# Kernel tuning notes

Hardware: AMD Instinct MI355X
Metric: run time of the kernel (lower is better)

The kernel has to match this reference:

```python
import jax, jax.numpy as jnp
import numpy as np

B, A, T, D, H, ATTN = 32, 128, 96, 16, 128, 64
MAX_DIST, EMB = 50, 32


def _ln(x, g, b, eps=1e-5):
    m = x.mean(-1, keepdims=True)
    v = ((x - m) ** 2).mean(-1, keepdims=True)
    return (x - m) / jnp.sqrt(v + eps) * g + b


def _lstm_layer(xs, Wih, Whh, bih, bhh):
    # xs: (N, T, Din); PyTorch gate order i, f, g, o
    n = xs.shape[0]
    h0 = jnp.zeros((n, Whh.shape[1]), xs.dtype)
    bias = bih + bhh
    def step(carry, x_t):
        h, c = carry
        gates = x_t @ Wih.T + h @ Whh.T + bias
        i, f, g, o = jnp.split(gates, 4, axis=-1)
        c = jax.nn.sigmoid(f) * c + jax.nn.sigmoid(i) * jnp.tanh(g)
        h = jax.nn.sigmoid(o) * jnp.tanh(c)
        return (h, c), h
    _, hs = jax.lax.scan(step, (h0, h0), jnp.swapaxes(xs, 0, 1))
    return jnp.swapaxes(hs, 0, 1)  # (N, T, H)


def _forward(ranks, x, W_ih0, W_hh0, b_ih0, b_hh0, W_ih1, W_hh1, b_ih1, b_hh1,
             attn_w, attn_W1, attn_W2, ln1_g, ln1_b, proj_W, proj_b,
             Wq, bq, Wk, bk, Wv, bv, rank_emb, rw1_W, rw1_b, rw2_W,
             ff1_W, ff1_b, ff2_W, ff2_b, ln2_g, ln2_b, sp1_W, sp1_b, sp2_W, sp2_b):
    b, a, t, d = x.shape
    xs = x.reshape(b * a, t, d)
    # LSTM-HA (dropout disabled, eval mode)
    h1 = _lstm_layer(xs, W_ih0, W_hh0, b_ih0, b_hh0)
    h2 = _lstm_layer(h1, W_ih1, W_hh1, b_ih1, b_hh1)
    hT = h2[:, -1, :]
    # additive history attention, vectorized over all timesteps
    alpha = jnp.tanh(h2 @ attn_W1 + (hT @ attn_W2)[:, None, :]) @ attn_w  # (b*a, t)
    w = jax.nn.softmax(alpha, axis=1)
    ctx = jnp.einsum('nt,nth->nh', w, h2)
    rep = _ln(ctx, ln1_g, ln1_b).reshape(b, a, -1)  # (b, a, H)
    # CAAN
    xp = rep @ proj_W + proj_b
    q = xp @ Wq + bq
    k = xp @ Wk + bk
    v = xp @ Wv + bv
    scores = jnp.einsum('bnd,bmd->bnm', q, k) / (ATTN ** 0.5)
    dist = jnp.clip(jnp.abs(ranks[:, :, None] - ranks[:, None, :]), 0, MAX_DIST)
    emb = rank_emb[dist]  # (b, a, a, EMB)
    gate = jax.nn.sigmoid(jax.nn.relu(emb @ rw1_W + rw1_b) @ rw2_W)  # (b, a, a)
    attn = jax.nn.softmax(scores * gate, axis=-1)
    ao = jnp.einsum('bnm,bmd->bnd', attn, v)
    ff = _ln(jax.nn.relu(ao @ ff1_W + ff1_b) @ ff2_W + ff2_b, ln2_g, ln2_b)
    return jax.nn.sigmoid((jax.nn.relu(ff @ sp1_W + sp1_b) @ sp2_W + sp2_b)[..., 0])


def setup_inputs() -> dict:
    key = jax.random.key(0)
    ks = jax.random.split(key, 40)
    it = iter(range(40))
    def rn(shape, s):
        return jax.random.normal(ks[next(it)], shape, jnp.float32) * s
    sH = 1.0 / float(np.sqrt(H))
    sA = 1.0 / float(np.sqrt(ATTN))
    return dict(
        x=jax.random.normal(ks[next(it)], (B, A, T, D), jnp.float32),
        ranks=jax.random.randint(ks[next(it)], (B, A), 0, A),
        W_ih0=rn((4 * H, D), sH), W_hh0=rn((4 * H, H), sH),
        b_ih0=jnp.zeros(4 * H), b_hh0=jnp.zeros(4 * H),
        W_ih1=rn((4 * H, H), sH), W_hh1=rn((4 * H, H), sH),
        b_ih1=jnp.zeros(4 * H), b_hh1=jnp.zeros(4 * H),
        attn_w=rn((H,), 0.06), attn_W1=rn((H, H), sH), attn_W2=rn((H, H), sH),
        ln1_g=jnp.ones(H), ln1_b=jnp.zeros(H),
        proj_W=rn((H, ATTN), sH), proj_b=jnp.zeros(ATTN),
        Wq=rn((ATTN, ATTN), sA), bq=jnp.zeros(ATTN),
        Wk=rn((ATTN, ATTN), sA), bk=jnp.zeros(ATTN),
        Wv=rn((ATTN, ATTN), sA), bv=jnp.zeros(ATTN),
        rank_emb=rn((MAX_DIST + 1, EMB), 1.0),
        rw1_W=rn((EMB, 16), 1.0 / float(np.sqrt(EMB))), rw1_b=jnp.zeros(16),
        rw2_W=rn((16,), 0.25),
        ff1_W=rn((ATTN, 2 * ATTN), sA), ff1_b=jnp.zeros(2 * ATTN),
        ff2_W=rn((2 * ATTN, ATTN), 1.0 / float(np.sqrt(2 * ATTN))), ff2_b=jnp.zeros(ATTN),
        ln2_g=jnp.ones(ATTN), ln2_b=jnp.zeros(ATTN),
        sp1_W=rn((ATTN, 32), sA), sp1_b=jnp.zeros(32),
        sp2_W=rn((32, 1), 0.18), sp2_b=jnp.zeros(1),
    )


def reference(x, ranks, W_ih0, W_hh0, b_ih0, b_hh0, W_ih1, W_hh1, b_ih1, b_hh1,
              attn_w, attn_W1, attn_W2, ln1_g, ln1_b, proj_W, proj_b,
              Wq, bq, Wk, bk, Wv, bv, rank_emb, rw1_W, rw1_b, rw2_W,
              ff1_W, ff1_b, ff2_W, ff2_b, ln2_g, ln2_b, sp1_W, sp1_b, sp2_W, sp2_b):
    return _forward(ranks, x, W_ih0, W_hh0, b_ih0, b_hh0, W_ih1, W_hh1, b_ih1, b_hh1,
                    attn_w, attn_W1, attn_W2, ln1_g, ln1_b, proj_W, proj_b,
                    Wq, bq, Wk, bk, Wv, bv, rank_emb, rw1_W, rw1_b, rw2_W,
                    ff1_W, ff1_b, ff2_W, ff2_b, ln2_g, ln2_b, sp1_W, sp1_b, sp2_W, sp2_b)
```

## Files before the change

kernel.cpp:

```cpp
#include <hip/hip_runtime.h>
#include <hip/hip_bf16.h>

namespace {

constexpr int T_ = 96;
constexpr int H_ = 128;

typedef short s8v __attribute__((ext_vector_type(8)));
typedef float f4v __attribute__((ext_vector_type(4)));

__device__ __forceinline__ float rcp_(float x) { return __builtin_amdgcn_rcpf(x); }
__device__ __forceinline__ float sig_(float x) { return rcp_(1.f + __expf(-x)); }
__device__ __forceinline__ float tanh_(float x) { return 1.f - 2.f * rcp_(__expf(2.f * x) + 1.f); }

__device__ __forceinline__ unsigned short bf16u(float f) {
  union { float f; unsigned u; } v; v.f = f;
  unsigned r = v.u + 0x7FFFu + ((v.u >> 16) & 1u);
  return (unsigned short)(r >> 16);
}
__device__ __forceinline__ float bf2f(unsigned short b) {
  union { unsigned u; float f; } v; v.u = ((unsigned)b) << 16;
  return v.f;
}

__device__ __forceinline__ s8v load8(const float* __restrict__ p) {
  const float4 a = *reinterpret_cast<const float4*>(p);
  const float4 b = *reinterpret_cast<const float4*>(p + 4);
  s8v r;
  r[0] = (short)bf16u(a.x); r[1] = (short)bf16u(a.y);
  r[2] = (short)bf16u(a.z); r[3] = (short)bf16u(a.w);
  r[4] = (short)bf16u(b.x); r[5] = (short)bf16u(b.y);
  r[6] = (short)bf16u(b.z); r[7] = (short)bf16u(b.w);
  return r;
}

__device__ __forceinline__ f4v mfma16(s8v a, s8v b, f4v c) {
  return __builtin_amdgcn_mfma_f32_16x16x32_bf16(a, b, c, 0, 0, 0);
}

__device__ __forceinline__ void barrier_lds() {
  __builtin_amdgcn_sched_barrier(0);
  asm volatile("s_waitcnt lgkmcnt(0)" ::: "memory");
  __builtin_amdgcn_s_barrier();
  __builtin_amdgcn_sched_barrier(0);
}

__global__ __launch_bounds__(64) void k0_gate(
    const float* __restrict__ remb,
    const float* __restrict__ rw1W, const float* __restrict__ rw1b,
    const float* __restrict__ rw2W,
    float* __restrict__ glut)
{
  const int d = threadIdx.x;
  if (d > 50) return;
  const float* er = remb + d * 32;
  float g = 0.f;
#pragma unroll
  for (int e = 0; e < 16; ++e) {
    float hs = rw1b[e];
#pragma unroll 8
    for (int i = 0; i < 32; ++i) hs += er[i] * rw1W[i * 16 + e];
    g += fmaxf(hs, 0.f) * rw2W[e];
  }
  glut[d] = sig_(g);
}

__global__ __launch_bounds__(256) void k0_w1(
    const float* __restrict__ W1, unsigned short* __restrict__ w1f)
{
  const int e = blockIdx.x * 256 + threadIdx.x;
  const int k = e >> 7, nn = e & 127;
  const int f = ((((nn >> 4) * 4 + (k >> 5)) * 4 + ((k >> 3) & 3)) * 16 + (nn & 15)) * 8 + (k & 7);
  w1f[f] = bf16u(W1[e]);
}

__global__ __launch_bounds__(256) void k0_whh1(
    const float* __restrict__ Whh1, unsigned short* __restrict__ whh1f)
{
  const int e = blockIdx.x * 256 + threadIdx.x;
  const int n = e >> 7, k = e & 127;
  const int g = n >> 7, wv = (n >> 4) & 7, l16 = n & 15;
  const int kt = k >> 5, lq = (k >> 3) & 3, i = k & 7;
  const int dst = (((g * 8 + wv) * 4 + kt) * 64 + lq * 16 + l16) * 8 + i;
  whh1f[dst] = bf16u(Whh1[e]);
}

__global__ __launch_bounds__(512) void k1_lstm_mfma(
    const float* __restrict__ x,
    const float* __restrict__ Wih0, const float* __restrict__ Whh0,
    const float* __restrict__ bih0, const float* __restrict__ bhh0,
    const float* __restrict__ Wih1, const float* __restrict__ whh1f,
    const float* __restrict__ bih1, const float* __restrict__ bhh1,
    unsigned short* __restrict__ hist)
{
  __shared__ __align__(16) unsigned short w1l[512 * 128];
  __shared__ __align__(16) unsigned short h1s[2][16 * 128];
  __shared__ __align__(16) unsigned short h2s[2][16 * 128];
  __shared__ __align__(16) unsigned short xb[2][16 * 32];

  const int tid  = threadIdx.x;
  const int lane = tid & 63;
  const int wv   = tid >> 6;
  const int l16  = lane & 15;
  const int lq   = lane >> 4;
  const int seqbase = blockIdx.x * 16;

  for (int i = tid; i < 2 * 16 * 128; i += 512) {
    (&h1s[0][0])[i] = 0; (&h2s[0][0])[i] = 0;
  }
  if (tid < 256) {
    const int s = tid >> 4, d = tid & 15;
    xb[0][s * 32 + 16 + d] = 0; xb[1][s * 32 + 16 + d] = 0;
    xb[0][s * 32 + d] = bf16u(x[((size_t)(seqbase + s) * T_ + 0) * 16 + d]);
  }
  {
    const uint4* src = reinterpret_cast<const uint4*>(whh1f);
    uint4* dst = reinterpret_cast<uint4*>(w1l);
    for (int i = tid; i < 8192; i += 512) dst[i] = src[i];
  }

  s8v whh0[4][4], wih1[4][4], wx0[4];
  float b0[4], b1[4];
  int wb[4];
#pragma unroll
  for (int g = 0; g < 4; ++g) {
    const int gr = g * 128 + 16 * wv + l16;
    b0[g] = bih0[gr] + bhh0[gr];
    b1[g] = bih1[gr] + bhh1[gr];
    wb[g] = ((g * 8 + wv) * 4) * 1024 + lane * 16;
#pragma unroll
    for (int kt = 0; kt < 4; ++kt) {
      const int k0 = kt * 32 + lq * 8;
      whh0[g][kt] = load8(Whh0 + (size_t)gr * 128 + k0);
      wih1[g][kt] = load8(Wih1 + (size_t)gr * 128 + k0);
    }
    if (lq < 2) wx0[g] = load8(Wih0 + (size_t)gr * 16 + lq * 8);
    else { s8v z; for (int i2 = 0; i2 < 8; ++i2) z[i2] = 0; wx0[g] = z; }
  }

  float c1[4] = {0.f, 0.f, 0.f, 0.f}, c2[4] = {0.f, 0.f, 0.f, 0.f};
  int cur = 0;
  __syncthreads();

  const int sw = (l16 & 7) << 4;
  const int hunit = 16 * wv + l16;

  for (int t = 0; t < T_; ++t) {
    const int xc = t & 1;
    float xv = 0.f;
    const bool xpf = (t + 1 < T_) && (tid < 256);
    if (xpf) {
      const int s = tid >> 4, d = tid & 15;
      xv = x[((size_t)(seqbase + s) * T_ + (t + 1)) * 16 + d];
    }

    f4v acc[4];
#pragma unroll
    for (int g = 0; g < 4; ++g) acc[g] = f4v{b0[g], b0[g], b0[g], b0[g]};
    {
      const s8v ax = *reinterpret_cast<const s8v*>(
          reinterpret_cast<const char*>(&xb[xc][0]) + l16 * 64 + lq * 16);
#pragma unroll
      for (int g = 0; g < 4; ++g) acc[g] = mfma16(ax, wx0[g], acc[g]);
    }
#pragma unroll
    for (int kt = 0; kt < 4; ++kt) {
      const s8v ah = *reinterpret_cast<const s8v*>(
          reinterpret_cast<const char*>(&h1s[cur][0]) + l16 * 256 +
          ((kt * 64 + lq * 16) ^ sw));
#pragma unroll
      for (int g = 0; g < 4; ++g) acc[g] = mfma16(ah, whh0[g][kt], acc[g]);
    }
#pragma unroll
    for (int ss = 0; ss < 4; ++ss) {
      const int seq = lq * 4 + ss;
      const float iv = sig_(acc[0][ss]);
      const float fv = sig_(acc[1][ss]);
      const float gv = tanh_(acc[2][ss]);
      const float ov = sig_(acc[3][ss]);
      c1[ss] = fv * c1[ss] + iv * gv;
      const float hv = ov * tanh_(c1[ss]);
      *reinterpret_cast<unsigned short*>(
          reinterpret_cast<char*>(&h1s[cur ^ 1][0]) + seq * 256 +
          ((2 * hunit) ^ ((seq & 7) << 4))) = bf16u(hv);
    }
    barrier_lds();

#pragma unroll
    for (int g = 0; g < 4; ++g) acc[g] = f4v{b1[g], b1[g], b1[g], b1[g]};
#pragma unroll
    for (int kt = 0; kt < 4; ++kt) {
      const int ko = (kt * 64 + lq * 16) ^ sw;
      const s8v a1 = *reinterpret_cast<const s8v*>(
          reinterpret_cast<const char*>(&h1s[cur ^ 1][0]) + l16 * 256 + ko);
      const s8v a2 = *reinterpret_cast<const s8v*>(
          reinterpret_cast<const char*>(&h2s[cur][0]) + l16 * 256 + ko);
#pragma unroll
      for (int g = 0; g < 4; ++g) {
        acc[g] = mfma16(a1, wih1[g][kt], acc[g]);
        const s8v bw = *reinterpret_cast<const s8v*>(
            reinterpret_cast<const char*>(w1l) + wb[g] + kt * 1024);
        acc[g] = mfma16(a2, bw, acc[g]);
      }
    }
#pragma unroll
    for (int ss = 0; ss < 4; ++ss) {
      const int seq = lq * 4 + ss;
      const float iv = sig_(acc[0][ss]);
      const float fv = sig_(acc[1][ss]);
      const float gv = tanh_(acc[2][ss]);
      const float ov = sig_(acc[3][ss]);
      c2[ss] = fv * c2[ss] + iv * gv;
      const float hv = ov * tanh_(c2[ss]);
      *reinterpret_cast<unsigned short*>(
          reinterpret_cast<char*>(&h2s[cur ^ 1][0]) + seq * 256 +
          ((2 * hunit) ^ ((seq & 7) << 4))) = bf16u(hv);
    }
    if (xpf) {
      const int s = tid >> 4, d = tid & 15;
      xb[xc ^ 1][s * 32 + d] = bf16u(xv);
    }
    barrier_lds();

    {
      const int seq = tid >> 5;
      const int u0  = (tid & 31) * 4;
      const uint2 v = *reinterpret_cast<const uint2*>(
          reinterpret_cast<const char*>(&h2s[cur ^ 1][0]) + seq * 256 +
          ((2 * u0) ^ ((seq & 7) << 4)));
      *reinterpret_cast<uint2*>(
          hist + ((size_t)(seqbase + seq) * T_ + t) * H_ + u0) = v;
    }
    cur ^= 1;
  }
}

__global__ __launch_bounds__(384, 2) void k2_pool_mfma(
    const unsigned short* __restrict__ hist,
    const unsigned short* __restrict__ w1f,
    const float* __restrict__ attn_w,
    const float* __restrict__ W2,
    const float* __restrict__ ln1g, const float* __restrict__ ln1b,
    float* __restrict__ rep)
{
  __shared__ __align__(16) unsigned short hst[96 * 128];
  __shared__ float sS[128], aws[128], alpha[96], wts[96], red[128], hTs[128];
  __shared__ float ctxP[3][128];

  const int n = blockIdx.x;
  const int tid = threadIdx.x;
  const int lane = tid & 63;
  const int wv = tid >> 6;
  const int l16 = lane & 15;
  const int lq = lane >> 4;

  const unsigned short* hsrc = hist + (size_t)n * T_ * H_;
  for (int i = tid; i < 1536; i += 384) {
    const int row = i >> 4, c16 = i & 15;
    const uint4 v = *reinterpret_cast<const uint4*>(hsrc + row * 128 + c16 * 8);
    *reinterpret_cast<uint4*>(
        reinterpret_cast<char*>(hst) + row * 256 + ((c16 * 16) ^ ((row & 7) << 4))) = v;
  }
  if (tid < 128) aws[tid] = attn_w[tid];
  __syncthreads();

  if (tid < 128) hTs[tid] = bf2f(hst[95 * 128 + (tid ^ 56)]);
  __syncthreads();
  if (tid < 128) {
    float s = 0.f;
    for (int h = 0; h < 128; ++h) s += hTs[h] * W2[(size_t)h * 128 + tid];
    sS[tid] = s;
  }
  __syncthreads();

  {
    const int row0 = wv * 16 + l16;
    f4v acc[8];
#pragma unroll
    for (int nt = 0; nt < 8; ++nt) acc[nt] = f4v{0.f, 0.f, 0.f, 0.f};
#pragma unroll
    for (int kt = 0; kt < 4; ++kt) {
      const s8v a = *reinterpret_cast<const s8v*>(
          reinterpret_cast<const char*>(hst) + row0 * 256 +
          ((kt * 64 + lq * 16) ^ ((row0 & 7) << 4)));
#pragma unroll
      for (int nt = 0; nt < 8; ++nt) {
        const s8v b = *reinterpret_cast<const s8v*>(
            w1f + ((((nt << 2) + kt) << 2 | lq) * 16 + l16) * 8);
        acc[nt] = mfma16(a, b, acc[nt]);
      }
    }
    float pa[4] = {0.f, 0.f, 0.f, 0.f};
#pragma unroll
    for (int nt = 0; nt < 8; ++nt) {
      const int col = nt * 16 + l16;
      const float ss = sS[col], aw = aws[col];
#pragma unroll
      for (int i2 = 0; i2 < 4; ++i2) pa[i2] += tanh_(acc[nt][i2] + ss) * aw;
    }
#pragma unroll
    for (int i2 = 0; i2 < 4; ++i2) {
      float v = pa[i2];
      v += __shfl_xor(v, 8); v += __shfl_xor(v, 4);
      v += __shfl_xor(v, 2); v += __shfl_xor(v, 1);
      if (l16 == 0) alpha[wv * 16 + lq * 4 + i2] = v;
    }
  }
  __syncthreads();

  if (tid < 128) red[tid] = (tid < 96) ? alpha[tid] : -1e30f;
  __syncthreads();
  for (int sft = 64; sft > 0; sft >>= 1) {
    if (tid < sft) red[tid] = fmaxf(red[tid], red[tid + sft]);
    __syncthreads();
  }
  const float mx = red[0];
  __syncthreads();
  if (tid < 128) {
    const float e = (tid < 96) ? __expf(alpha[tid] - mx) : 0.f;
    red[tid] = e;
    if (tid < 96) wts[tid] = e;
  }
  __syncthreads();
  for (int sft = 64; sft > 0; sft >>= 1) {
    if (tid < sft) red[tid] += red[tid + sft];
    __syncthreads();
  }
  const float inv = rcp_(red[0]);
  if (tid < 96) wts[tid] *= inv;
  __syncthreads();

  {
    const int th = tid >> 7, j = tid & 127;
    float cp = 0.f;
    for (int t = th * 32; t < th * 32 + 32; ++t)
      cp += wts[t] * bf2f(hst[t * 128 + (j ^ ((t & 7) << 3))]);
    ctxP[th][j] = cp;
  }
  __syncthreads();
  if (tid < 128) {
    hTs[tid] = ctxP[0][tid] + ctxP[1][tid] + ctxP[2][tid];
    red[tid] = hTs[tid];
  }
  __syncthreads();
  for (int sft = 64; sft > 0; sft >>= 1) {
    if (tid < sft) red[tid] += red[tid + sft];
    __syncthreads();
  }
  const float mean = red[0] * (1.f / 128.f);
  __syncthreads();
  if (tid < 128) { const float d = hTs[tid] - mean; red[tid] = d * d; }
  __syncthreads();
  for (int sft = 64; sft > 0; sft >>= 1) {
    if (tid < sft) red[tid] += red[tid + sft];
    __syncthreads();
  }
  const float var = red[0] * (1.f / 128.f);
  if (tid < 128)
    rep[(size_t)n * H_ + tid] =
        (hTs[tid] - mean) * rsqrtf(var + 1e-5f) * ln1g[tid] + ln1b[tid];
}

__global__ __launch_bounds__(256) void k3_qkv(
    const float* __restrict__ rep,
    const float* __restrict__ projW, const float* __restrict__ projb,
    const float* __restrict__ Wq, const float* __restrict__ bq,
    const float* __restrict__ Wk, const float* __restrict__ bk,
    const float* __restrict__ Wv, const float* __restrict__ bv,
    float* __restrict__ q, float* __restrict__ k, float* __restrict__ v)
{
  const int rbase = blockIdx.x * 32;
  const int tid = threadIdx.x;
  __shared__ float reps[32][128];
  __shared__ float xps[32][64];
  for (int i = tid; i < 32 * 128; i += 256)
    reps[i >> 7][i & 127] = rep[(size_t)(rbase + (i >> 7)) * 128 + (i & 127)];
  __syncthreads();
  const int col = tid & 63, rg = tid >> 6;
#pragma unroll 2
  for (int rr = 0; rr < 8; ++rr) {
    const int r = rg * 8 + rr;
    float acc = projb[col];
    for (int kk = 0; kk < 128; ++kk) acc += reps[r][kk] * projW[kk * 64 + col];
    xps[r][col] = acc;
  }
  __syncthreads();
#pragma unroll 2
  for (int rr = 0; rr < 8; ++rr) {
    const int r = rg * 8 + rr;
    float aq = bq[col], ak = bk[col], av = bv[col];
    for (int kk = 0; kk < 64; ++kk) {
      const float xv = xps[r][kk];
      aq += xv * Wq[kk * 64 + col];
      ak += xv * Wk[kk * 64 + col];
      av += xv * Wv[kk * 64 + col];
    }
    const size_t o = (size_t)(rbase + r) * 64 + col;
    q[o] = aq; k[o] = ak; v[o] = av;
  }
}

__global__ __launch_bounds__(128) void k4_attn(
    const float* __restrict__ q, const float* __restrict__ kbuf, const float* __restrict__ vbuf,
    const int* __restrict__ ranks, const float* __restrict__ glut,
    float* __restrict__ ao)
{
  const int bn = blockIdx.x;
  const int b = bn >> 7;
  const int m = threadIdx.x;
  __shared__ float qs[64], attnw[128], red[128], aoP[2][64], gl[51];
  if (m < 64) qs[m] = q[(size_t)bn * 64 + m];
  if (m >= 64 && m < 64 + 51) gl[m - 64] = glut[m - 64];
  __syncthreads();
  const float* kr = kbuf + (size_t)(b * 128 + m) * 64;
  float sc = 0.f;
#pragma unroll 8
  for (int d = 0; d < 64; ++d) sc += qs[d] * kr[d];
  sc *= 0.125f;
  const int rn = ranks[bn], rm = ranks[b * 128 + m];
  int dist = rn - rm;
  if (dist < 0) dist = -dist;
  if (dist > 50) dist = 50;
  const float smv = sc * gl[dist];
  red[m] = smv;
  __syncthreads();
  for (int sft = 64; sft > 0; sft >>= 1) {
    if (m < sft) red[m] = fmaxf(red[m], red[m + sft]);
    __syncthreads();
  }
  const float mx = red[0];
  __syncthreads();
  const float e = __expf(smv - mx);
  red[m] = e;
  __syncthreads();
  for (int sft = 64; sft > 0; sft >>= 1) {
    if (m < sft) red[m] += red[m + sft];
    __syncthreads();
  }
  attnw[m] = e / red[0];
  __syncthreads();
  const int d = m & 63, half = m >> 6;
  float acc = 0.f;
  for (int mm = half * 64; mm < half * 64 + 64; ++mm)
    acc += attnw[mm] * vbuf[(size_t)(b * 128 + mm) * 64 + d];
  aoP[half][d] = acc;
  __syncthreads();
  if (m < 64) ao[(size_t)bn * 64 + m] = aoP[0][m] + aoP[1][m];
}

__global__ __launch_bounds__(128) void k5_ffout(
    const float* __restrict__ ao,
    const float* __restrict__ ff1W, const float* __restrict__ ff1b,
    const float* __restrict__ ff2W, const float* __restrict__ ff2b,
    const float* __restrict__ ln2g, const float* __restrict__ ln2b,
    const float* __restrict__ sp1W, const float* __restrict__ sp1b,
    const float* __restrict__ sp2W, const float* __restrict__ sp2b,
    float* __restrict__ out)
{
  const int row = blockIdx.x;
  const int tid = threadIdx.x;
  __shared__ float aos[64], hid[128], ffs[64], red[128], h2b[32];
  if (tid < 64) aos[tid] = ao[(size_t)row * 64 + tid];
  __syncthreads();
  float hv = ff1b[tid];
  for (int dd = 0; dd < 64; ++dd) hv += aos[dd] * ff1W[dd * 128 + tid];
  hid[tid] = fmaxf(hv, 0.f);
  __syncthreads();
  float yv = 0.f;
  if (tid < 64) {
    yv = ff2b[tid];
    for (int h2 = 0; h2 < 128; ++h2) yv += hid[h2] * ff2W[h2 * 64 + tid];
  }
  red[tid] = (tid < 64) ? yv : 0.f;
  __syncthreads();
  for (int sft = 64; sft > 0; sft >>= 1) {
    if (tid < sft) red[tid] += red[tid + sft];
    __syncthreads();
  }
  const float mean = red[0] * (1.f / 64.f);
  __syncthreads();
  {
    const float d2 = (tid < 64) ? (yv - mean) : 0.f;
    red[tid] = d2 * d2;
  }
  __syncthreads();
  for (int sft = 64; sft > 0; sft >>= 1) {
    if (tid < sft) red[tid] += red[tid + sft];
    __syncthreads();
  }
  const float var = red[0] * (1.f / 64.f);
  __syncthreads();
  if (tid < 64) ffs[tid] = (yv - mean) * rsqrtf(var + 1e-5f) * ln2g[tid] + ln2b[tid];
  __syncthreads();
  if (tid < 32) {
    float h2v = sp1b[tid];
    for (int c = 0; c < 64; ++c) h2v += ffs[c] * sp1W[c * 32 + tid];
    h2b[tid] = fmaxf(h2v, 0.f);
  }
  __syncthreads();
  if (tid == 0) {
    float o = sp2b[0];
#pragma unroll
    for (int e2 = 0; e2 < 32; ++e2) o += h2b[e2] * sp2W[e2];
    out[row] = sig_(o);
  }
}

}

extern "C" void kernel_launch(void* const* d_in, const int* in_sizes, int n_in,
                              void* d_out, int out_size, void* d_ws, size_t ws_size,
                              hipStream_t stream)
{
  const float* x      = (const float*)d_in[0];
  const int*   ranks  = (const int*)  d_in[1];
  const float* Wih0   = (const float*)d_in[2];
  const float* Whh0   = (const float*)d_in[3];
  const float* bih0   = (const float*)d_in[4];
  const float* bhh0   = (const float*)d_in[5];
  const float* Wih1   = (const float*)d_in[6];
  const float* Whh1   = (const float*)d_in[7];
  const float* bih1   = (const float*)d_in[8];
  const float* bhh1   = (const float*)d_in[9];
  const float* attn_w = (const float*)d_in[10];
  const float* W1     = (const float*)d_in[11];
  const float* W2     = (const float*)d_in[12];
  const float* ln1g   = (const float*)d_in[13];
  const float* ln1b   = (const float*)d_in[14];
  const float* projW  = (const float*)d_in[15];
  const float* projb  = (const float*)d_in[16];
  const float* Wq     = (const float*)d_in[17];
  const float* bq     = (const float*)d_in[18];
  const float* Wk     = (const float*)d_in[19];
  const float* bk     = (const float*)d_in[20];
  const float* Wv     = (const float*)d_in[21];
  const float* bv     = (const float*)d_in[22];
  const float* remb   = (const float*)d_in[23];
  const float* rw1W   = (const float*)d_in[24];
  const float* rw1b   = (const float*)d_in[25];
  const float* rw2W   = (const float*)d_in[26];
  const float* ff1W   = (const float*)d_in[27];
  const float* ff1b   = (const float*)d_in[28];
  const float* ff2W   = (const float*)d_in[29];
  const float* ff2b   = (const float*)d_in[30];
  const float* ln2g   = (const float*)d_in[31];
  const float* ln2b   = (const float*)d_in[32];
  const float* sp1W   = (const float*)d_in[33];
  const float* sp1b   = (const float*)d_in[34];
  const float* sp2W   = (const float*)d_in[35];
  const float* sp2b   = (const float*)d_in[36];
  float* out = (float*)d_out;

  char* ws = (char*)d_ws;
  unsigned short* hist = (unsigned short*)ws;
  size_t off = (size_t)4096 * 96 * 128 * 2;
  float* rep = (float*)(ws + off); off += (size_t)4096 * 128 * 4;
  float* qb  = (float*)(ws + off); off += (size_t)4096 * 64 * 4;
  float* kb  = (float*)(ws + off); off += (size_t)4096 * 64 * 4;
  float* vb  = (float*)(ws + off); off += (size_t)4096 * 64 * 4;
  float* aob = (float*)(ws + off); off += (size_t)4096 * 64 * 4;
  unsigned short* w1f   = (unsigned short*)(ws + off); off += 16384 * 2;
  float* glut = (float*)(ws + off); off += 64 * 4;
  unsigned short* whh1f = (unsigned short*)(ws + off); off += 65536 * 2;

  k0_gate<<<dim3(1), dim3(64), 0, stream>>>(remb, rw1W, rw1b, rw2W, glut);
  k0_w1<<<dim3(64), dim3(256), 0, stream>>>(W1, w1f);
  k0_whh1<<<dim3(256), dim3(256), 0, stream>>>(Whh1, whh1f);
  k1_lstm_mfma<<<dim3(256), dim3(512), 0, stream>>>(
      x, Wih0, Whh0, bih0, bhh0, Wih1, (const float*)whh1f, bih1, bhh1, hist);
  k2_pool_mfma<<<dim3(4096), dim3(384), 0, stream>>>(
      hist, w1f, attn_w, W2, ln1g, ln1b, rep);
  k3_qkv<<<dim3(128), dim3(256), 0, stream>>>(
      rep, projW, projb, Wq, bq, Wk, bk, Wv, bv, qb, kb, vb);
  k4_attn<<<dim3(4096), dim3(128), 0, stream>>>(
      qb, kb, vb, ranks, glut, aob);
  k5_ffout<<<dim3(4096), dim3(128), 0, stream>>>(
      aob, ff1W, ff1b, ff2W, ff2b, ln2g, ln2b, sp1W, sp1b, sp2W, sp2b, out);
}
```

Measured before the change: 422.4 us.

## Pipeline LSTM layers across two wavefront groups with one barrier per step

The LSTM kernel now launches 1024 threads split into two groups of eight waves. One group runs layer 0 at step i while the other runs layer 1 at step i-1, using double-buffered h1/h2 in LDS. This removes one of the two block barriers per timestep and lets the two layers' MFMA and activation work overlap. Each group keeps only its own layer's weights in registers. The cost is a doubled block size, which may limit occupancy and raise per-barrier cost, plus an extra pipeline step and a tail write for the final hidden state.

```diff
diff --git a/kernel.cpp b/kernel.cpp
--- a/kernel.cpp
+++ b/kernel.cpp
@@ -79,13 +79,13 @@
 {
   const int e = blockIdx.x * 256 + threadIdx.x;
   const int n = e >> 7, k = e & 127;
-  const int g = n >> 7, wv = (n >> 4) & 7, l16 = n & 15;
+  const int g = n >> 7, wl = (n >> 4) & 7, l16 = n & 15;
   const int kt = k >> 5, lq = (k >> 3) & 3, i = k & 7;
-  const int dst = (((g * 8 + wv) * 4 + kt) * 64 + lq * 16 + l16) * 8 + i;
+  const int dst = (((g * 8 + wl) * 4 + kt) * 64 + lq * 16 + l16) * 8 + i;
   whh1f[dst] = bf16u(Whh1[e]);
 }
 
-__global__ __launch_bounds__(512) void k1_lstm_mfma(
+__global__ __launch_bounds__(1024) void k1_lstm_pipe(
     const float* __restrict__ x,
     const float* __restrict__ Wih0, const float* __restrict__ Whh0,
     const float* __restrict__ bih0, const float* __restrict__ bhh0,
@@ -101,11 +101,13 @@
   const int tid  = threadIdx.x;
   const int lane = tid & 63;
   const int wv   = tid >> 6;
+  const int grp  = wv >> 3;
+  const int wl   = wv & 7;
   const int l16  = lane & 15;
   const int lq   = lane >> 4;
   const int seqbase = blockIdx.x * 16;
 
-  for (int i = tid; i < 2 * 16 * 128; i += 512) {
+  for (int i = tid; i < 2 * 16 * 128; i += 1024) {
     (&h1s[0][0])[i] = 0; (&h2s[0][0])[i] = 0;
   }
   if (tid < 256) {
@@ -116,122 +118,133 @@
   {
     const uint4* src = reinterpret_cast<const uint4*>(whh1f);
     uint4* dst = reinterpret_cast<uint4*>(w1l);
-    for (int i = tid; i < 8192; i += 512) dst[i] = src[i];
-  }
-
-  s8v whh0[4][4], wih1[4][4], wx0[4];
-  float b0[4], b1[4];
+    for (int i = tid; i < 8192; i += 1024) dst[i] = src[i];
+  }
+
+  s8v frag[4][4], wx0[4];
+  float bias[4];
+  float c[4] = {0.f, 0.f, 0.f, 0.f};
   int wb[4];
 #pragma unroll
   for (int g = 0; g < 4; ++g) {
-    const int gr = g * 128 + 16 * wv + l16;
-    b0[g] = bih0[gr] + bhh0[gr];
-    b1[g] = bih1[gr] + bhh1[gr];
-    wb[g] = ((g * 8 + wv) * 4) * 1024 + lane * 16;
-#pragma unroll
-    for (int kt = 0; kt < 4; ++kt) {
-      const int k0 = kt * 32 + lq * 8;
-      whh0[g][kt] = load8(Whh0 + (size_t)gr * 128 + k0);
-      wih1[g][kt] = load8(Wih1 + (size_t)gr * 128 + k0);
+    const int gr = g * 128 + 16 * wl + l16;
+    if (grp == 0) {
+      bias[g] = bih0[gr] + bhh0[gr];
+#pragma unroll
+      for (int kt = 0; kt < 4; ++kt)
+        frag[g][kt] = load8(Whh0 + (size_t)gr * 128 + kt * 32 + lq * 8);
+      if (lq < 2) wx0[g] = load8(Wih0 + (size_t)gr * 16 + lq * 8);
+      else { s8v z; for (int i2 = 0; i2 < 8; ++i2) z[i2] = 0; wx0[g] = z; }
+      wb[g] = 0;
+    } else {
+      bias[g] = bih1[gr] + bhh1[gr];
+#pragma unroll
+      for (int kt = 0; kt < 4; ++kt)
+        frag[g][kt] = load8(Wih1 + (size_t)gr * 128 + kt * 32 + lq * 8);
+      wb[g] = ((g * 8 + wl) * 4) * 1024 + lane * 16;
     }
-    if (lq < 2) wx0[g] = load8(Wih0 + (size_t)gr * 16 + lq * 8);
-    else { s8v z; for (int i2 = 0; i2 < 8; ++i2) z[i2] = 0; wx0[g] = z; }
-  }
-
-  float c1[4] = {0.f, 0.f, 0.f, 0.f}, c2[4] = {0.f, 0.f, 0.f, 0.f};
-  int cur = 0;
+  }
   __syncthreads();
 
   const int sw = (l16 & 7) << 4;
-  const int hunit = 16 * wv + l16;
-
-  for (int t = 0; t < T_; ++t) {
-    const int xc = t & 1;
-    float xv = 0.f;
-    const bool xpf = (t + 1 < T_) && (tid < 256);
-    if (xpf) {
-      const int s = tid >> 4, d = tid & 15;
-      xv = x[((size_t)(seqbase + s) * T_ + (t + 1)) * 16 + d];
-    }
-
-    f4v acc[4];
-#pragma unroll
-    for (int g = 0; g < 4; ++g) acc[g] = f4v{b0[g], b0[g], b0[g], b0[g]};
-    {
-      const s8v ax = *reinterpret_cast<const s8v*>(
-          reinterpret_cast<const char*>(&xb[xc][0]) + l16 * 64 + lq * 16);
-#pragma unroll
-      for (int g = 0; g < 4; ++g) acc[g] = mfma16(ax, wx0[g], acc[g]);
-    }
-#pragma unroll
-    for (int kt = 0; kt < 4; ++kt) {
-      const s8v ah = *reinterpret_cast<const s8v*>(
-          reinterpret_cast<const char*>(&h1s[cur][0]) + l16 * 256 +
-          ((kt * 64 + lq * 16) ^ sw));
-#pragma unroll
-      for (int g = 0; g < 4; ++g) acc[g] = mfma16(ah, whh0[g][kt], acc[g]);
-    }
-#pragma unroll
-    for (int ss = 0; ss < 4; ++ss) {
-      const int seq = lq * 4 + ss;
-      const float iv = sig_(acc[0][ss]);
-      const float fv = sig_(acc[1][ss]);
-      const float gv = tanh_(acc[2][ss]);
-      const float ov = sig_(acc[3][ss]);
-      c1[ss] = fv * c1[ss] + iv * gv;
-      const float hv = ov * tanh_(c1[ss]);
-      *reinterpret_cast<unsigned short*>(
-          reinterpret_cast<char*>(&h1s[cur ^ 1][0]) + seq * 256 +
-          ((2 * hunit) ^ ((seq & 7) << 4))) = bf16u(hv);
+  const int hunit = 16 * wl + l16;
+
+  for (int i = 0; i <= T_; ++i) {
+    const int cb = i & 1;
+    if (grp == 0) {
+      if (i >= 2) {
+        const int seq = tid >> 5;
+        const int u0  = (tid & 31) * 4;
+        const uint2 v = *reinterpret_cast<const uint2*>(
+            reinterpret_cast<const char*>(&h2s[cb][0]) + seq * 256 +
+            ((2 * u0) ^ ((seq & 7) << 4)));
+        *reinterpret_cast<uint2*>(
+            hist + ((size_t)(seqbase + seq) * T_ + (i - 2)) * H_ + u0) = v;
+      }
+      if (i < T_) {
+        float xv = 0.f; int xs = 0, xd = 0;
+        const bool xpf = (i < T_ - 1) && (tid < 256);
+        if (xpf) {
+          xs = tid >> 4; xd = tid & 15;
+          xv = x[((size_t)(seqbase + xs) * T_ + (i + 1)) * 16 + xd];
+        }
+        f4v acc[4];
+#pragma unroll
+        for (int g = 0; g < 4; ++g) acc[g] = f4v{bias[g], bias[g], bias[g], bias[g]};
+        {
+          const s8v ax = *reinterpret_cast<const s8v*>(
+              reinterpret_cast<const char*>(&xb[cb][0]) + l16 * 64 + lq * 16);
+#pragma unroll
+          for (int g = 0; g < 4; ++g) acc[g] = mfma16(ax, wx0[g], acc[g]);
+        }
+#pragma unroll
+        for (int kt = 0; kt < 4; ++kt) {
+          const s8v ah = *reinterpret_cast<const s8v*>(
+              reinterpret_cast<const char*>(&h1s[cb][0]) + l16 * 256 +
+              ((kt * 64 + lq * 16) ^ sw));
+#pragma unroll
+          for (int g = 0; g < 4; ++g) acc[g] = mfma16(ah, frag[g][kt], acc[g]);
+        }
+#pragma unroll
+        for (int ss = 0; ss < 4; ++ss) {
+          const int seq = lq * 4 + ss;
+          const float iv = sig_(acc[0][ss]);
+          const float fv = sig_(acc[1][ss]);
+          const float gv = tanh_(acc[2][ss]);
+          const float ov = sig_(acc[3][ss]);
+          c[ss] = fv * c[ss] + iv * gv;
+          const float hv = ov * tanh_(c[ss]);
+          *reinterpret_cast<unsigned short*>(
+              reinterpret_cast<char*>(&h1s[cb ^ 1][0]) + seq * 256 +
+              ((2 * hunit) ^ ((seq & 7) << 4))) = bf16u(hv);
+        }
+        if (xpf) xb[cb ^ 1][xs * 32 + xd] = bf16u(xv);
+      }
+    } else {
+      if (i >= 1) {
+        f4v acc[4];
+#pragma unroll
+        for (int g = 0; g < 4; ++g) acc[g] = f4v{bias[g], bias[g], bias[g], bias[g]};
+#pragma unroll
+        for (int kt = 0; kt < 4; ++kt) {
+          const int ko = (kt * 64 + lq * 16) ^ sw;
+          const s8v a1 = *reinterpret_cast<const s8v*>(
+              reinterpret_cast<const char*>(&h1s[cb][0]) + l16 * 256 + ko);
+          const s8v a2 = *reinterpret_cast<const s8v*>(
+              reinterpret_cast<const char*>(&h2s[cb][0]) + l16 * 256 + ko);
+#pragma unroll
+          for (int g = 0; g < 4; ++g) {
+            acc[g] = mfma16(a1, frag[g][kt], acc[g]);
+            const s8v bw = *reinterpret_cast<const s8v*>(
+                reinterpret_cast<const char*>(w1l) + wb[g] + kt * 1024);
+            acc[g] = mfma16(a2, bw, acc[g]);
+          }
+        }
+#pragma unroll
+        for (int ss = 0; ss < 4; ++ss) {
+          const int seq = lq * 4 + ss;
+          const float iv = sig_(acc[0][ss]);
+          const float fv = sig_(acc[1][ss]);
+          const float gv = tanh_(acc[2][ss]);
+          const float ov = sig_(acc[3][ss]);
+          c[ss] = fv * c[ss] + iv * gv;
+          const float hv = ov * tanh_(c[ss]);
+          *reinterpret_cast<unsigned short*>(
+              reinterpret_cast<char*>(&h2s[cb ^ 1][0]) + seq * 256 +
+              ((2 * hunit) ^ ((seq & 7) << 4))) = bf16u(hv);
+        }
+      }
     }
     barrier_lds();
-
-#pragma unroll
-    for (int g = 0; g < 4; ++g) acc[g] = f4v{b1[g], b1[g], b1[g], b1[g]};
-#pragma unroll
-    for (int kt = 0; kt < 4; ++kt) {
-      const int ko = (kt * 64 + lq * 16) ^ sw;
-      const s8v a1 = *reinterpret_cast<const s8v*>(
-          reinterpret_cast<const char*>(&h1s[cur ^ 1][0]) + l16 * 256 + ko);
-      const s8v a2 = *reinterpret_cast<const s8v*>(
-          reinterpret_cast<const char*>(&h2s[cur][0]) + l16 * 256 + ko);
-#pragma unroll
-      for (int g = 0; g < 4; ++g) {
-        acc[g] = mfma16(a1, wih1[g][kt], acc[g]);
-        const s8v bw = *reinterpret_cast<const s8v*>(
-            reinterpret_cast<const char*>(w1l) + wb[g] + kt * 1024);
-        acc[g] = mfma16(a2, bw, acc[g]);
-      }
-    }
-#pragma unroll
-    for (int ss = 0; ss < 4; ++ss) {
-      const int seq = lq * 4 + ss;
-      const float iv = sig_(acc[0][ss]);
-      const float fv = sig_(acc[1][ss]);
-      const float gv = tanh_(acc[2][ss]);
-      const float ov = sig_(acc[3][ss]);
-      c2[ss] = fv * c2[ss] + iv * gv;
-      const float hv = ov * tanh_(c2[ss]);
-      *reinterpret_cast<unsigned short*>(
-          reinterpret_cast<char*>(&h2s[cur ^ 1][0]) + seq * 256 +
-          ((2 * hunit) ^ ((seq & 7) << 4))) = bf16u(hv);
-    }
-    if (xpf) {
-      const int s = tid >> 4, d = tid & 15;
-      xb[xc ^ 1][s * 32 + d] = bf16u(xv);
-    }
-    barrier_lds();
-
-    {
-      const int seq = tid >> 5;
-      const int u0  = (tid & 31) * 4;
-      const uint2 v = *reinterpret_cast<const uint2*>(
-          reinterpret_cast<const char*>(&h2s[cur ^ 1][0]) + seq * 256 +
-          ((2 * u0) ^ ((seq & 7) << 4)));
-      *reinterpret_cast<uint2*>(
-          hist + ((size_t)(seqbase + seq) * T_ + t) * H_ + u0) = v;
-    }
-    cur ^= 1;
+  }
+  if (tid < 512) {
+    const int seq = tid >> 5;
+    const int u0  = (tid & 31) * 4;
+    const uint2 v = *reinterpret_cast<const uint2*>(
+        reinterpret_cast<const char*>(&h2s[1][0]) + seq * 256 +
+        ((2 * u0) ^ ((seq & 7) << 4)));
+    *reinterpret_cast<uint2*>(
+        hist + ((size_t)(seqbase + seq) * T_ + (T_ - 1)) * H_ + u0) = v;
   }
 }
 
@@ -566,7 +579,7 @@
   k0_gate<<<dim3(1), dim3(64), 0, stream>>>(remb, rw1W, rw1b, rw2W, glut);
   k0_w1<<<dim3(64), dim3(256), 0, stream>>>(W1, w1f);
   k0_whh1<<<dim3(256), dim3(256), 0, stream>>>(Whh1, whh1f);
-  k1_lstm_mfma<<<dim3(256), dim3(512), 0, stream>>>(
+  k1_lstm_pipe<<<dim3(256), dim3(1024), 0, stream>>>(
       x, Wih0, Whh0, bih0, bhh0, Wih1, (const float*)whh1f, bih1, bhh1, hist);
   k2_pool_mfma<<<dim3(4096), dim3(384), 0, stream>>>(
       hist, w1f, attn_w, W2, ln1g, ln1b, rep);
```

Measured after the change: 690.2 us. 1.63x slower.

## Tile CAAN attention per batch chunk with LDS-resident K/V and wave softmax

Applied to the files above, without the earlier changes.

Replaces the per-query-row attention kernel (4096 blocks of 128 threads) with 256 blocks of 512 threads. Each block loads one batch's full K and V into padded shared memory and handles 16 query rows, two rows per wave. Softmax reductions now use wave shuffles instead of shared-memory tree reductions with repeated block barriers. The aim is to cut redundant global K/V reads and barrier overhead, in exchange for about 66KB of LDS per block, lower occupancy and fewer blocks. Within a wave, the writes to the shared weight row are ordered against the later reads only by an s_waitcnt, with no barrier.

```diff
diff --git a/kernel.cpp b/kernel.cpp
--- a/kernel.cpp
+++ b/kernel.cpp
@@ -79,9 +79,9 @@
 {
   const int e = blockIdx.x * 256 + threadIdx.x;
   const int n = e >> 7, k = e & 127;
-  const int g = n >> 7, wv = (n >> 4) & 7, l16 = n & 15;
+  const int g = n >> 7, wl = (n >> 4) & 7, l16 = n & 15;
   const int kt = k >> 5, lq = (k >> 3) & 3, i = k & 7;
-  const int dst = (((g * 8 + wv) * 4 + kt) * 64 + lq * 16 + l16) * 8 + i;
+  const int dst = (((g * 8 + wl) * 4 + kt) * 64 + lq * 16 + l16) * 8 + i;
   whh1f[dst] = bf16u(Whh1[e]);
 }
 
@@ -400,52 +400,64 @@
   }
 }
 
-__global__ __launch_bounds__(128) void k4_attn(
-    const float* __restrict__ q, const float* __restrict__ kbuf, const float* __restrict__ vbuf,
+__global__ __launch_bounds__(512) void k4_attn_b(
+    const float* __restrict__ q, const float* __restrict__ kbuf,
+    const float* __restrict__ vbuf,
     const int* __restrict__ ranks, const float* __restrict__ glut,
     float* __restrict__ ao)
 {
-  const int bn = blockIdx.x;
-  const int b = bn >> 7;
-  const int m = threadIdx.x;
-  __shared__ float qs[64], attnw[128], red[128], aoP[2][64], gl[51];
-  if (m < 64) qs[m] = q[(size_t)bn * 64 + m];
-  if (m >= 64 && m < 64 + 51) gl[m - 64] = glut[m - 64];
-  __syncthreads();
-  const float* kr = kbuf + (size_t)(b * 128 + m) * 64;
-  float sc = 0.f;
+  __shared__ float Ks[128][65], Vs[128][65];
+  __shared__ float qs[16][64];
+  __shared__ float wrow[8][128];
+  __shared__ float gl[51];
+  __shared__ int rs[128];
+
+  const int tid = threadIdx.x, lane = tid & 63, wv = tid >> 6;
+  const int b = blockIdx.x >> 3;
+  const int rowbase = (blockIdx.x & 7) * 16;
+
+  for (int i = tid; i < 8192; i += 512) {
+    Ks[i >> 6][i & 63] = kbuf[(size_t)b * 8192 + i];
+    Vs[i >> 6][i & 63] = vbuf[(size_t)b * 8192 + i];
+  }
+  for (int i = tid; i < 1024; i += 512)
+    qs[i >> 6][i & 63] = q[((size_t)b * 128 + rowbase) * 64 + i];
+  if (tid < 128) rs[tid] = ranks[b * 128 + tid];
+  if (tid >= 128 && tid < 179) gl[tid - 128] = glut[tid - 128];
+  __syncthreads();
+
+  const int m0 = lane, m1 = lane + 64;
+#pragma unroll
+  for (int rr = 0; rr < 2; ++rr) {
+    const int lr = wv * 2 + rr;
+    const int rn = rs[rowbase + lr];
+    float s0 = 0.f, s1 = 0.f;
 #pragma unroll 8
-  for (int d = 0; d < 64; ++d) sc += qs[d] * kr[d];
-  sc *= 0.125f;
-  const int rn = ranks[bn], rm = ranks[b * 128 + m];
-  int dist = rn - rm;
-  if (dist < 0) dist = -dist;
-  if (dist > 50) dist = 50;
-  const float smv = sc * gl[dist];
-  red[m] = smv;
-  __syncthreads();
-  for (int sft = 64; sft > 0; sft >>= 1) {
-    if (m < sft) red[m] = fmaxf(red[m], red[m + sft]);
-    __syncthreads();
-  }
-  const float mx = red[0];
-  __syncthreads();
-  const float e = __expf(smv - mx);
-  red[m] = e;
-  __syncthreads();
-  for (int sft = 64; sft > 0; sft >>= 1) {
-    if (m < sft) red[m] += red[m + sft];
-    __syncthreads();
-  }
-  attnw[m] = e / red[0];
-  __syncthreads();
-  const int d = m & 63, half = m >> 6;
-  float acc = 0.f;
-  for (int mm = half * 64; mm < half * 64 + 64; ++mm)
-    acc += attnw[mm] * vbuf[(size_t)(b * 128 + mm) * 64 + d];
-  aoP[half][d] = acc;
-  __syncthreads();
-  if (m < 64) ao[(size_t)bn * 64 + m] = aoP[0][m] + aoP[1][m];
+    for (int d = 0; d < 64; ++d) {
+      const float qd = qs[lr][d];
+      s0 += qd * Ks[m0][d];
+      s1 += qd * Ks[m1][d];
+    }
+    int d0 = rn - rs[m0]; if (d0 < 0) d0 = -d0; if (d0 > 50) d0 = 50;
+    int d1 = rn - rs[m1]; if (d1 < 0) d1 = -d1; if (d1 > 50) d1 = 50;
+    s0 *= 0.125f * gl[d0];
+    s1 *= 0.125f * gl[d1];
+    float mx = fmaxf(s0, s1);
+#pragma unroll
+    for (int off = 32; off; off >>= 1) mx = fmaxf(mx, __shfl_xor(mx, off));
+    const float e0 = __expf(s0 - mx), e1 = __expf(s1 - mx);
+    float sum = e0 + e1;
+#pragma unroll
+    for (int off = 32; off; off >>= 1) sum += __shfl_xor(sum, off);
+    const float inv = rcp_(sum);
+    wrow[wv][m0] = e0 * inv;
+    wrow[wv][m1] = e1 * inv;
+    asm volatile("s_waitcnt lgkmcnt(0)" ::: "memory");
+    float acc = 0.f;
+#pragma unroll 4
+    for (int m = 0; m < 128; ++m) acc += wrow[wv][m] * Vs[m][lane];
+    ao[((size_t)b * 128 + rowbase + lr) * 64 + lane] = acc;
+  }
 }
 
 __global__ __launch_bounds__(128) void k5_ffout(
@@ -572,7 +584,7 @@
       hist, w1f, attn_w, W2, ln1g, ln1b, rep);
   k3_qkv<<<dim3(128), dim3(256), 0, stream>>>(
       rep, projW, projb, Wq, bq, Wk, bk, Wv, bv, qb, kb, vb);
-  k4_attn<<<dim3(4096), dim3(128), 0, stream>>>(
+  k4_attn_b<<<dim3(256), dim3(512), 0, stream>>>(
       qb, kb, vb, ranks, glut, aob);
   k5_ffout<<<dim3(4096), dim3(128), 0, stream>>>(
       aob, ff1W, ff1b, ff2W, ff2b, ln2g, ln2b, sp1W, sp1b, sp2W, sp2b, out);
```

New measurement: 399.0 us. 5.5% less time.
